# Performance work log

Hardware: AMD Instinct MI355X
Metric: run time of the kernel (lower is better)

The kernel has to match this reference:

```python
import jax, jax.numpy as jnp
import numpy as np

B, S, D_IN, D_OUT, H = 2, 2048, 1024, 1024, 16
DK = D_OUT // H


def setup_inputs() -> dict:
    key = jax.random.key(0)
    ks = jax.random.split(key, 6)
    s_in = 1.0 / np.sqrt(D_IN)
    s_out = 1.0 / np.sqrt(D_OUT)
    return {
        "x": jax.random.normal(ks[0], (B, S, D_IN), dtype=jnp.float32),
        "Wq": jax.random.uniform(ks[1], (D_OUT, D_IN), jnp.float32, -s_in, s_in),
        "Wk": jax.random.uniform(ks[2], (D_OUT, D_IN), jnp.float32, -s_in, s_in),
        "Wv": jax.random.uniform(ks[3], (D_OUT, D_IN), jnp.float32, -s_in, s_in),
        "Wo": jax.random.uniform(ks[4], (D_OUT, D_OUT), jnp.float32, -s_out, s_out),
        "bo": jax.random.uniform(ks[5], (D_OUT,), jnp.float32, -s_out, s_out),
    }


def reference(x, Wq, Wk, Wv, Wo, bo):
    b, s, _ = x.shape
    # torch Linear: y = x @ W.T
    q = (x @ Wq.T).reshape(b, s, H, DK).transpose(0, 2, 1, 3)  # [b,h,s,dk]
    k = (x @ Wk.T).reshape(b, s, H, DK).transpose(0, 2, 1, 3)
    v = (x @ Wv.T).reshape(b, s, H, DK).transpose(0, 2, 1, 3)
    scores = jnp.einsum("bhqd,bhkd->bhqk", q, k)
    causal = jnp.tril(jnp.ones((s, s), dtype=bool))  # True = keep
    scores = jnp.where(causal, scores, -jnp.inf)
    attn = jax.nn.softmax(scores / np.sqrt(DK), axis=-1)
    # dropout p=0.0 (eval) -> identity
    ctx = jnp.einsum("bhqk,bhkd->bhqd", attn, v)
    ctx = ctx.transpose(0, 2, 1, 3).reshape(b, s, D_OUT)
    return ctx @ Wo.T + bo
```

## Files before the change

kernel.cpp:

```cpp
#include <hip/hip_runtime.h>
#include <stdint.h>

#define B_   2
#define S_   2048
#define DIN  1024
#define DOUT 1024
#define H_   16
#define DK_  64
#define MSZ  (B_ * S_)

typedef __bf16 bf16v8 __attribute__((ext_vector_type(8)));
typedef float  f32x4  __attribute__((ext_vector_type(4)));

__device__ __forceinline__ ushort f2b(float f) {
  union { float f; uint32_t u; } a; a.f = f;
  uint32_t u = a.u;
  u += 0x7FFFu + ((u >> 16) & 1u);
  return (ushort)(u >> 16);
}

__device__ __forceinline__ uint32_t pk2(float lo, float hi) {
  union { __bf16 h; ushort u; } a, b;
  a.h = (__bf16)lo; b.h = (__bf16)hi;
  return (uint32_t)a.u | ((uint32_t)b.u << 16);
}

#define GLDS(gp, lp) __builtin_amdgcn_global_load_lds(                         \
    (const __attribute__((address_space(1))) void*)(gp),                       \
    (__attribute__((address_space(3))) void*)(lp), 16, 0, 0)

__global__ void cvt_all(const float* __restrict__ x,  const float* __restrict__ wq,
                        const float* __restrict__ wk, const float* __restrict__ wv,
                        const float* __restrict__ wo,
                        ushort* __restrict__ xb,  ushort* __restrict__ wqb,
                        ushort* __restrict__ wkb, ushort* __restrict__ wvb,
                        ushort* __restrict__ wob) {
  int i = blockIdx.x * blockDim.x + threadIdx.x;
  const int NX = 1 << 20, NW = 1 << 18;
  const float* src; ushort* dst; int off;
  if (i < NX)               { src = x;  dst = xb;  off = i; }
  else if (i < NX + NW)     { src = wq; dst = wqb; off = i - NX; }
  else if (i < NX + 2 * NW) { src = wk; dst = wkb; off = i - NX - NW; }
  else if (i < NX + 3 * NW) { src = wv; dst = wvb; off = i - NX - 2 * NW; }
  else                      { src = wo; dst = wob; off = i - NX - 3 * NW; }
  float4 v = reinterpret_cast<const float4*>(src)[off];
  ushort4 o;
  o.x = f2b(v.x); o.y = f2b(v.y); o.z = f2b(v.z); o.w = f2b(v.w);
  reinterpret_cast<ushort4*>(dst)[off] = o;
}

template<int MODE>
__global__ __launch_bounds__(256)
void gemm_nt(const ushort* __restrict__ A,
             const ushort* __restrict__ Bq, const ushort* __restrict__ Bk,
             const ushort* __restrict__ Bv,
             ushort* __restrict__ Oq, ushort* __restrict__ Ok,
             ushort* __restrict__ Vt,
             float* __restrict__ Cf, const float* __restrict__ bias,
             int M, int N, int K) {
  __shared__ ushort sA[128 * 32];
  __shared__ ushort sB[128 * 32];

  const int tid  = threadIdx.x;
  const int lane = tid & 63, wid = tid >> 6;
  const int wr = wid >> 1, wc = wid & 1;
  const int g = lane >> 4, c = lane & 15;
  const int m0 = blockIdx.x * 128, n0 = blockIdx.y * 128;

  const ushort* Bm = Bq;
  ushort* Ob = nullptr;
  float oscale = 1.0f;
  bool tv = false;
  if (MODE == 0) {
    int z = blockIdx.z;
    Bm = (z == 0) ? Bq : (z == 1) ? Bk : Bv;
    Ob = (z == 0) ? Oq : Ok;
    tv = (z == 2);
    if (z == 0) oscale = 0.125f * 1.4426950408889634f;
  }

  f32x4 acc[4][4] = {};

  for (int k0 = 0; k0 < K; k0 += 32) {
    __syncthreads();
#pragma unroll
    for (int i = 0; i < 2; ++i) {
      int o   = (i * 256 + tid) * 16;
      int row = o >> 6;
      int cb  = o & 63;
      const ushort* ga = A  + (size_t)(m0 + row) * K + k0 + (cb >> 1);
      GLDS(ga, (char*)sA + o);
      const ushort* gb = Bm + (size_t)(n0 + row) * K + k0 + (cb >> 1);
      GLDS(gb, (char*)sB + o);
    }
    __syncthreads();

    bf16v8 aF[4], bF[4];
#pragma unroll
    for (int m = 0; m < 4; ++m)
      aF[m] = *reinterpret_cast<const bf16v8*>(&sA[(wr * 64 + m * 16 + c) * 32 + g * 8]);
#pragma unroll
    for (int n = 0; n < 4; ++n)
      bF[n] = *reinterpret_cast<const bf16v8*>(&sB[(wc * 64 + n * 16 + c) * 32 + g * 8]);
#pragma unroll
    for (int m = 0; m < 4; ++m)
#pragma unroll
      for (int n = 0; n < 4; ++n)
        acc[m][n] = __builtin_amdgcn_mfma_f32_16x16x32_bf16(aF[m], bF[n], acc[m][n], 0, 0, 0);
  }

  const int rbase = m0 + wr * 64 + g * 4;
  const int cbase = n0 + wc * 64 + c;
#pragma unroll
  for (int m = 0; m < 4; ++m) {
#pragma unroll
    for (int n = 0; n < 4; ++n) {
      int col = cbase + n * 16;
      if (MODE == 1) {
        float bv = bias[col];
#pragma unroll
        for (int i = 0; i < 4; ++i)
          Cf[(size_t)(rbase + m * 16 + i) * N + col] = acc[m][n][i] + bv;
      } else if (tv) {
        int row0 = rbase + m * 16;
        int bb = row0 >> 11, ss = row0 & 2047;
        int hh = col >> 6, dd = col & 63;
        ushort4 o4;
        o4.x = f2b(acc[m][n][0]); o4.y = f2b(acc[m][n][1]);
        o4.z = f2b(acc[m][n][2]); o4.w = f2b(acc[m][n][3]);
        *reinterpret_cast<ushort4*>(
            &Vt[((size_t)(bb * 16 + hh) * 64 + dd) * 2048 + ss]) = o4;
      } else {
#pragma unroll
        for (int i = 0; i < 4; ++i)
          Ob[(size_t)(rbase + m * 16 + i) * N + col] = f2b(acc[m][n][i] * oscale);
      }
    }
  }
}

__global__ __launch_bounds__(512)
void flash_attn(const ushort* __restrict__ Q, const ushort* __restrict__ K,
                const ushort* __restrict__ Vt, ushort* __restrict__ O) {
  __shared__ ushort sK[2][64][64];
  __shared__ ushort sV[2][64][64];
  __shared__ ushort sP[8][16][64];

  const int tid  = threadIdx.x;
  const int lane = tid & 63, wid = tid >> 6;
  const int wid4 = wid & 3;
  const int g = lane >> 4, c = lane & 15;

  const int orig = blockIdx.x;
  const int xcd  = orig & 7, idc = orig >> 3;
  const int bh   = xcd * 4 + (idc >> 4);
  const int tp   = idc & 15;
  const int b = bh >> 4, h = bh & 15;
  const int q0    = (wid < 4) ? tp * 64 : (31 - tp) * 64;
  const int q0max = (31 - tp) * 64;

  const ushort* Qb = Q  + (size_t)b * S_ * DOUT + h * DK_;
  const ushort* Kb = K  + (size_t)b * S_ * DOUT + h * DK_;
  const ushort* Vb = Vt + (size_t)bh * DK_ * S_;

  const int srow = tid >> 3;
  const int swc  = ((tid & 7) ^ (srow & 7)) << 3;
  const int msk  = (c & 7) << 4;
  const int pswz = (c & 7) << 2;

  bf16v8 qf[2];
  {
    const ushort* qrow = Qb + (size_t)(q0 + wid4 * 16 + c) * DOUT;
    qf[0] = *reinterpret_cast<const bf16v8*>(qrow + g * 8);
    qf[1] = *reinterpret_cast<const bf16v8*>(qrow + 32 + g * 8);
  }

  bf16v8 ones;
#pragma unroll
  for (int j = 0; j < 8; ++j) ones[j] = (__bf16)1.0f;

  GLDS(Kb + (size_t)srow * DOUT + swc, (char*)&sK[0][0][0] + tid * 16);
  GLDS(Vb + (size_t)srow * S_  + swc, (char*)&sV[0][0][0] + tid * 16);
  __syncthreads();

  f32x4 accO[4] = {};
  f32x4 accL = {};
  char* sPw = (char*)&sP[wid][0][0];
  const int qg = q0 + wid4 * 16 + c;
  const int qdiag = q0 + wid4 * 16;

  int buf = 0;
  for (int kv0 = 0; kv0 <= q0max; kv0 += 64, buf ^= 1) {
    if (kv0 + 64 <= q0max) {
      const int nb = buf ^ 1, kvn = kv0 + 64;
      GLDS(Kb + (size_t)(kvn + srow) * DOUT + swc,
           (char*)&sK[nb][0][0] + tid * 16);
      GLDS(Vb + (size_t)srow * S_ + kvn + swc,
           (char*)&sV[nb][0][0] + tid * 16);
    }

    if (kv0 <= q0) {
      const char* cK = (const char*)&sK[buf][0][0];
      const char* cV = (const char*)&sV[buf][0][0];

      f32x4 s[4] = {};
      __builtin_amdgcn_s_setprio(1);
#pragma unroll
      for (int nf = 0; nf < 4; ++nf) {
        const char* rp = cK + (nf * 16 + c) * 128;
#pragma unroll
        for (int ks = 0; ks < 2; ++ks) {
          bf16v8 kf = *reinterpret_cast<const bf16v8*>(rp + ((ks * 64 + g * 16) ^ msk));
          s[nf] = __builtin_amdgcn_mfma_f32_16x16x32_bf16(kf, qf[ks], s[nf], 0, 0, 0);
        }
      }
      __builtin_amdgcn_s_setprio(0);

      if (kv0 + 63 > qdiag) {
#pragma unroll
        for (int nf = 0; nf < 4; ++nf)
#pragma unroll
          for (int i = 0; i < 4; ++i)
            if (kv0 + nf * 16 + g * 4 + i > qg) s[nf][i] = -1e30f;
      }

#pragma unroll
      for (int nf = 0; nf < 4; ++nf) {
        float p0 = exp2f(s[nf][0]), p1 = exp2f(s[nf][1]);
        float p2 = exp2f(s[nf][2]), p3 = exp2f(s[nf][3]);
        uint2 w2; w2.x = pk2(p0, p1); w2.y = pk2(p2, p3);
        *reinterpret_cast<uint2*>(
            sPw + c * 128 + (((nf * 8 + g * 2) ^ pswz) << 2)) = w2;
      }
      bf16v8 pf[2];
#pragma unroll
      for (int ks = 0; ks < 2; ++ks)
        pf[ks] = *reinterpret_cast<const bf16v8*>(
            sPw + c * 128 + (((ks * 16 + g * 4) ^ pswz) << 2));

      __builtin_amdgcn_s_setprio(1);
#pragma unroll
      for (int ks = 0; ks < 2; ++ks)
        accL = __builtin_amdgcn_mfma_f32_16x16x32_bf16(pf[ks], ones, accL, 0, 0, 0);
#pragma unroll
      for (int nf2 = 0; nf2 < 4; ++nf2) {
        const char* vp = cV + (nf2 * 16 + c) * 128;
#pragma unroll
        for (int ks = 0; ks < 2; ++ks) {
          bf16v8 vf = *reinterpret_cast<const bf16v8*>(vp + ((ks * 64 + g * 16) ^ msk));
          accO[nf2] = __builtin_amdgcn_mfma_f32_16x16x32_bf16(pf[ks], vf, accO[nf2], 0, 0, 0);
        }
      }
      __builtin_amdgcn_s_setprio(0);
    }

    __syncthreads();
  }

#pragma unroll
  for (int nf = 0; nf < 4; ++nf)
#pragma unroll
    for (int i = 0; i < 4; ++i) {
      int prow = g * 4 + i;
      float v = accO[nf][i] / accL[i];
      *(ushort*)(sPw + prow * 128 +
                 ((nf * 32 + c * 2) ^ ((prow & 7) << 4))) = f2b(v);
    }
  {
    const int r = lane >> 2, cq = lane & 3;
    const char* base = sPw + r * 128;
    const int m2 = (r & 7) << 4;
    bf16v8 t0 = *reinterpret_cast<const bf16v8*>(base + ((cq * 32) ^ m2));
    bf16v8 t1 = *reinterpret_cast<const bf16v8*>(base + ((cq * 32 + 16) ^ m2));
    ushort* Gb = O + (size_t)b * S_ * DOUT +
                 (size_t)(q0 + wid4 * 16 + r) * DOUT + h * DK_ + cq * 16;
    *reinterpret_cast<bf16v8*>(Gb) = t0;
    *reinterpret_cast<bf16v8*>(Gb + 8) = t1;
  }
}

extern "C" void kernel_launch(void* const* d_in, const int* in_sizes, int n_in,
                              void* d_out, int out_size, void* d_ws, size_t ws_size,
                              hipStream_t stream) {
  const float* x  = (const float*)d_in[0];
  const float* Wq = (const float*)d_in[1];
  const float* Wk = (const float*)d_in[2];
  const float* Wv = (const float*)d_in[3];
  const float* Wo = (const float*)d_in[4];
  const float* bo = (const float*)d_in[5];
  float* out = (float*)d_out;

  char* ws = (char*)d_ws;
  const size_t MB = (size_t)1 << 20;
  ushort* xb  = (ushort*)(ws);
  ushort* wqb = (ushort*)(ws +  8 * MB);
  ushort* wkb = (ushort*)(ws + 10 * MB);
  ushort* wvb = (ushort*)(ws + 12 * MB);
  ushort* wob = (ushort*)(ws + 14 * MB);
  ushort* qb  = (ushort*)(ws + 16 * MB);
  ushort* kb  = (ushort*)(ws + 24 * MB);
  ushort* vtb = (ushort*)(ws + 32 * MB);
  ushort* cb  = (ushort*)(ws);

  const int ncv = (1 << 20) + 4 * (1 << 18);
  cvt_all<<<ncv / 256, 256, 0, stream>>>(x, Wq, Wk, Wv, Wo,
                                         xb, wqb, wkb, wvb, wob);

  dim3 gqkv(MSZ / 128, DOUT / 128, 3);
  gemm_nt<0><<<gqkv, 256, 0, stream>>>(xb, wqb, wkb, wvb, qb, kb, vtb,
                                       nullptr, nullptr, MSZ, DOUT, DIN);

  flash_attn<<<B_ * H_ * (S_ / 128), 512, 0, stream>>>(qb, kb, vtb, cb);

  dim3 gproj(MSZ / 128, DOUT / 128, 1);
  gemm_nt<1><<<gproj, 256, 0, stream>>>(cb, wob, nullptr, nullptr,
                                        nullptr, nullptr, nullptr, out, bo,
                                        MSZ, DOUT, DOUT);
}
```

Measured before the change: 119.9 us.

## Deepen GEMM K-tile to 64 with XOR-swizzled LDS and staged coalesced epilogue

The QKV and output-projection GEMMs now load 64-wide K slices per iteration, halving the number of barrier-separated iterations. The shared-memory tiles use an XOR swizzle to avoid bank conflicts on fragment reads. The Q/K and fp32 output epilogues are staged through LDS so each lane writes 16-byte vectors instead of scattered 2- or 4-byte stores. The grid is also flattened from a z dimension into y. The cost is doubled LDS per block, which may reduce occupancy, plus an extra LDS round trip in the epilogue.

```diff
diff --git a/kernel.cpp b/kernel.cpp
--- a/kernel.cpp
+++ b/kernel.cpp
@@ -57,72 +57,77 @@
              ushort* __restrict__ Oq, ushort* __restrict__ Ok,
              ushort* __restrict__ Vt,
              float* __restrict__ Cf, const float* __restrict__ bias,
-             int M, int N, int K) {
-  __shared__ ushort sA[128 * 32];
-  __shared__ ushort sB[128 * 32];
+             int M, int K) {
+  __shared__ ushort sA[128 * 64];
+  __shared__ ushort sB[128 * 64];
 
   const int tid  = threadIdx.x;
   const int lane = tid & 63, wid = tid >> 6;
   const int wr = wid >> 1, wc = wid & 1;
   const int g = lane >> 4, c = lane & 15;
-  const int m0 = blockIdx.x * 128, n0 = blockIdx.y * 128;
-
-  const ushort* Bm = Bq;
-  ushort* Ob = nullptr;
-  float oscale = 1.0f;
-  bool tv = false;
+  const int m0 = blockIdx.x * 128;
+
+  int wsel = 0, n0w = blockIdx.y * 128;
+  const ushort* Bm;
   if (MODE == 0) {
-    int z = blockIdx.z;
-    Bm = (z == 0) ? Bq : (z == 1) ? Bk : Bv;
-    Ob = (z == 0) ? Oq : Ok;
-    tv = (z == 2);
-    if (z == 0) oscale = 0.125f * 1.4426950408889634f;
-  }
+    wsel = blockIdx.y >> 3;
+    n0w  = (blockIdx.y & 7) * 128;
+    Bm = (wsel == 0) ? Bq : (wsel == 1) ? Bk : Bv;
+  } else {
+    Bm = Bq;
+  }
+
+  const int msk = (c & 7) << 4;
 
   f32x4 acc[4][4] = {};
 
-  for (int k0 = 0; k0 < K; k0 += 32) {
+  for (int k0 = 0; k0 < K; k0 += 64) {
     __syncthreads();
 #pragma unroll
-    for (int i = 0; i < 2; ++i) {
-      int o   = (i * 256 + tid) * 16;
-      int row = o >> 6;
-      int cb  = o & 63;
-      const ushort* ga = A  + (size_t)(m0 + row) * K + k0 + (cb >> 1);
-      GLDS(ga, (char*)sA + o);
-      const ushort* gb = Bm + (size_t)(n0 + row) * K + k0 + (cb >> 1);
-      GLDS(gb, (char*)sB + o);
+    for (int i = 0; i < 4; ++i) {
+      int idx = i * 256 + tid;
+      int row = idx >> 3;
+      int scol = (((idx & 7) ^ (row & 7)) << 3);
+      GLDS(A  + (size_t)(m0 + row) * K + k0 + scol,
+           (char*)sA + idx * 16);
+      GLDS(Bm + (size_t)(n0w + row) * K + k0 + scol,
+           (char*)sB + idx * 16);
     }
     __syncthreads();
 
-    bf16v8 aF[4], bF[4];
+    bf16v8 aF[4][2], bF[4][2];
+#pragma unroll
+    for (int m = 0; m < 4; ++m) {
+      const char* rp = (const char*)sA + (wr * 64 + m * 16 + c) * 128;
+#pragma unroll
+      for (int ks = 0; ks < 2; ++ks)
+        aF[m][ks] = *reinterpret_cast<const bf16v8*>(rp + ((ks * 64 + g * 16) ^ msk));
+    }
+#pragma unroll
+    for (int n = 0; n < 4; ++n) {
+      const char* rp = (const char*)sB + (wc * 64 + n * 16 + c) * 128;
+#pragma unroll
+      for (int ks = 0; ks < 2; ++ks)
+        bF[n][ks] = *reinterpret_cast<const bf16v8*>(rp + ((ks * 64 + g * 16) ^ msk));
+    }
 #pragma unroll
     for (int m = 0; m < 4; ++m)
-      aF[m] = *reinterpret_cast<const bf16v8*>(&sA[(wr * 64 + m * 16 + c) * 32 + g * 8]);
-#pragma unroll
-    for (int n = 0; n < 4; ++n)
-      bF[n] = *reinterpret_cast<const bf16v8*>(&sB[(wc * 64 + n * 16 + c) * 32 + g * 8]);
+#pragma unroll
+      for (int n = 0; n < 4; ++n) {
+        acc[m][n] = __builtin_amdgcn_mfma_f32_16x16x32_bf16(aF[m][0], bF[n][0], acc[m][n], 0, 0, 0);
+        acc[m][n] = __builtin_amdgcn_mfma_f32_16x16x32_bf16(aF[m][1], bF[n][1], acc[m][n], 0, 0, 0);
+      }
+  }
+
+  __syncthreads();
+
+  if (MODE == 0 && wsel == 2) {
 #pragma unroll
     for (int m = 0; m < 4; ++m)
 #pragma unroll
-      for (int n = 0; n < 4; ++n)
-        acc[m][n] = __builtin_amdgcn_mfma_f32_16x16x32_bf16(aF[m], bF[n], acc[m][n], 0, 0, 0);
-  }
-
-  const int rbase = m0 + wr * 64 + g * 4;
-  const int cbase = n0 + wc * 64 + c;
-#pragma unroll
-  for (int m = 0; m < 4; ++m) {
-#pragma unroll
-    for (int n = 0; n < 4; ++n) {
-      int col = cbase + n * 16;
-      if (MODE == 1) {
-        float bv = bias[col];
-#pragma unroll
-        for (int i = 0; i < 4; ++i)
-          Cf[(size_t)(rbase + m * 16 + i) * N + col] = acc[m][n][i] + bv;
-      } else if (tv) {
-        int row0 = rbase + m * 16;
+      for (int n = 0; n < 4; ++n) {
+        int row0 = m0 + wr * 64 + g * 4 + m * 16;
+        int col  = n0w + wc * 64 + c + n * 16;
         int bb = row0 >> 11, ss = row0 & 2047;
         int hh = col >> 6, dd = col & 63;
         ushort4 o4;
@@ -130,10 +135,52 @@
         o4.z = f2b(acc[m][n][2]); o4.w = f2b(acc[m][n][3]);
         *reinterpret_cast<ushort4*>(
             &Vt[((size_t)(bb * 16 + hh) * 64 + dd) * 2048 + ss]) = o4;
-      } else {
-#pragma unroll
-        for (int i = 0; i < 4; ++i)
-          Ob[(size_t)(rbase + m * 16 + i) * N + col] = f2b(acc[m][n][i] * oscale);
+      }
+  } else if (MODE == 0) {
+    const float oscale = (wsel == 0) ? 0.125f * 1.4426950408889634f : 1.0f;
+    ushort* Ob = (wsel == 0) ? Oq : Ok;
+    char* eb = (char*)sA + wid * 2048;
+#pragma unroll
+    for (int m = 0; m < 4; ++m) {
+#pragma unroll
+      for (int n = 0; n < 4; ++n)
+#pragma unroll
+        for (int i = 0; i < 4; ++i) {
+          int prow = g * 4 + i;
+          *(ushort*)(eb + prow * 128 + ((n * 32 + c * 2) ^ ((prow & 7) << 4))) =
+              f2b(acc[m][n][i] * oscale);
+        }
+      const int r = lane >> 2, cq = lane & 3;
+      const int m2 = (r & 7) << 4;
+      bf16v8 t0 = *reinterpret_cast<const bf16v8*>(eb + r * 128 + ((cq * 32) ^ m2));
+      bf16v8 t1 = *reinterpret_cast<const bf16v8*>(eb + r * 128 + ((cq * 32 + 16) ^ m2));
+      ushort* Gb = Ob + (size_t)(m0 + wr * 64 + m * 16 + r) * DOUT +
+                   n0w + wc * 64 + cq * 16;
+      *reinterpret_cast<bf16v8*>(Gb) = t0;
+      *reinterpret_cast<bf16v8*>(Gb + 8) = t1;
+    }
+  } else {
+    float bv[4];
+#pragma unroll
+    for (int n = 0; n < 4; ++n) bv[n] = bias[n0w + wc * 64 + n * 16 + c];
+    float* ef = (float*)((char*)sA + wid * 4096);
+#pragma unroll
+    for (int m = 0; m < 4; ++m) {
+#pragma unroll
+      for (int n = 0; n < 4; ++n)
+#pragma unroll
+        for (int i = 0; i < 4; ++i) {
+          int prow = g * 4 + i;
+          ef[prow * 64 + ((n * 16 + c) ^ ((prow & 12) << 2))] = acc[m][n][i] + bv[n];
+        }
+      const int r = lane >> 2, q = lane & 3;
+      const int mk = (r & 12) << 2;
+#pragma unroll
+      for (int k = 0; k < 4; ++k) {
+        float4 v = *reinterpret_cast<const float4*>(&ef[r * 64 + ((q * 16 + k * 4) ^ mk)]);
+        *reinterpret_cast<float4*>(
+            &Cf[(size_t)(m0 + wr * 64 + m * 16 + r) * DOUT +
+                n0w + wc * 64 + q * 16 + k * 4]) = v;
       }
     }
   }
@@ -306,14 +353,14 @@
   cvt_all<<<ncv / 256, 256, 0, stream>>>(x, Wq, Wk, Wv, Wo,
                                          xb, wqb, wkb, wvb, wob);
 
-  dim3 gqkv(MSZ / 128, DOUT / 128, 3);
+  dim3 gqkv(MSZ / 128, 24, 1);
   gemm_nt<0><<<gqkv, 256, 0, stream>>>(xb, wqb, wkb, wvb, qb, kb, vtb,
-                                       nullptr, nullptr, MSZ, DOUT, DIN);
+                                       nullptr, nullptr, MSZ, DIN);
 
   flash_attn<<<B_ * H_ * (S_ / 128), 512, 0, stream>>>(qb, kb, vtb, cb);
 
   dim3 gproj(MSZ / 128, DOUT / 128, 1);
   gemm_nt<1><<<gproj, 256, 0, stream>>>(cb, wob, nullptr, nullptr,
                                         nullptr, nullptr, nullptr, out, bo,
-                                        MSZ, DOUT, DOUT);
-}
+                                        MSZ, DOUT);
+}
```

New measurement: 117.4 us. 2.1% less time.
